# Performance work log

Hardware: AMD Instinct MI355X
Metric: run time of the kernel (lower is better)

Reference implementation:

```python
import jax, jax.numpy as jnp
import numpy as np

INPUT_SIZE = 608
STRIDE = 32
NUM_CLASSES = 20
NMS_THRESH = 0.5
NUM_ANCHOR = 5
ANCHORS = np.array([[1.19, 1.98], [2.79, 4.59], [4.53, 8.92], [8.06, 5.29], [10.32, 10.65]], dtype=np.float32)


def _conv(x, w, b, pad):
    # x: NCHW, w: OIHW
    y = jax.lax.conv_general_dilated(x, w, (1, 1), [(pad, pad), (pad, pad)],
                                     dimension_numbers=('NCHW', 'OIHW', 'NCHW'))
    return y + b[None, :, None, None]


def _leaky(x):
    return jnp.where(x > 0, x, 0.1 * x)


def _reorg(x, s=2):
    # space-to-depth, darknet reorg: [B,C,H,W] -> [B,C*s*s,H/s,W/s]
    B, C, H, W = x.shape
    x = x.reshape(B, C, H // s, s, W // s, s)
    x = x.transpose(0, 3, 5, 1, 2, 4)
    return x.reshape(B, C * s * s, H // s, W // s)


def _forward_boxes_scores(feat_layer2, feat_layer3, w1a, b1a, w1b, b1b, wr, br, w2, b2, wp, bp):
    p5 = _leaky(_conv(feat_layer3, w1a, b1a, 1))
    p5 = _leaky(_conv(p5, w1b, b1b, 1))
    p4 = _reorg(_leaky(_conv(feat_layer2, wr, br, 0)))         # [1,256,19,19]
    p5 = jnp.concatenate([p4, p5], axis=1)                      # [1,1280,19,19]
    p5 = _leaky(_conv(p5, w2, b2, 1))
    pred = _conv(p5, wp, bp, 0)                                 # [1,125,19,19]
    B, C, H, W = pred.shape
    pred = pred.transpose(0, 2, 3, 1).reshape(B, H * W, C)
    conf = pred[:, :, :NUM_ANCHOR].reshape(B, H * W * NUM_ANCHOR, 1)
    cls = pred[:, :, NUM_ANCHOR:(1 + NUM_CLASSES) * NUM_ANCHOR].reshape(B, H * W * NUM_ANCHOR, NUM_CLASSES)
    reg = pred[:, :, (1 + NUM_CLASSES) * NUM_ANCHOR:].reshape(B, H * W, NUM_ANCHOR, 4)
    # decode_xywh
    gy, gx = jnp.meshgrid(jnp.arange(H), jnp.arange(W), indexing='ij')
    grid = jnp.stack([gx, gy], axis=-1).astype(pred.dtype).reshape(1, H * W, 1, 2)
    anchor_wh = jnp.asarray(ANCHORS).reshape(1, 1, NUM_ANCHOR, 2)
    xy = jax.nn.sigmoid(reg[..., :2]) + grid
    wh = jnp.exp(reg[..., 2:]) * anchor_wh
    xywh = jnp.concatenate([xy, wh], axis=-1).reshape(B, -1, 4) * STRIDE
    boxes = jnp.concatenate([xywh[..., :2] - 0.5 * xywh[..., 2:],
                             xywh[..., :2] + 0.5 * xywh[..., 2:]], axis=-1)
    boxes = jnp.clip(boxes[0] / INPUT_SIZE, 0.0, 1.0)           # [N,4]
    scores = jax.nn.sigmoid(conf[0]) * jax.nn.softmax(cls[0], axis=-1)  # [N,20]
    return boxes, scores


def _per_class_nms(boxes, scores, class_mask):
    # greedy sequential NMS, faithful to the torch while-loop (suppress iff IoU > thresh)
    N = boxes.shape[0]
    s = jnp.where(class_mask, scores, -jnp.inf)
    order = jnp.argsort(-s)
    b = boxes[order]
    valid = class_mask[order]
    x1, y1, x2, y2 = b[:, 0], b[:, 1], b[:, 2], b[:, 3]
    areas = (x2 - x1) * (y2 - y1)
    iw = jnp.maximum(1e-10, jnp.minimum(x2[:, None], x2[None, :]) - jnp.maximum(x1[:, None], x1[None, :]))
    ih = jnp.maximum(1e-10, jnp.minimum(y2[:, None], y2[None, :]) - jnp.maximum(y1[:, None], y1[None, :]))
    inter = iw * ih
    iou = inter / (areas[:, None] + areas[None, :] - inter)
    upper = jnp.arange(N)[None, :] > jnp.arange(N)[:, None]
    sup_mat = (iou > NMS_THRESH) & upper

    def body(i, state):
        suppressed, keep = state
        cur = valid[i] & jnp.logical_not(suppressed[i])
        keep = keep.at[i].set(cur)
        suppressed = suppressed | (cur & sup_mat[i])
        return suppressed, keep

    _, keep_sorted = jax.lax.fori_loop(0, N, body, (jnp.zeros(N, bool), jnp.zeros(N, bool)))
    return jnp.zeros(N, bool).at[order].set(keep_sorted)


def setup_inputs() -> dict:
    key = jax.random.key(0)
    ks = jax.random.split(key, 8)
    w = lambda k, shape: jax.random.normal(k, shape, jnp.float32) * 0.01
    return {
        'feat_layer2': jax.random.normal(ks[0], (1, 512, 38, 38), jnp.float32),
        'feat_layer3': jax.random.normal(ks[1], (1, 1024, 19, 19), jnp.float32),
        'w1a': w(ks[2], (1024, 1024, 3, 3)), 'b1a': jnp.zeros((1024,), jnp.float32),
        'w1b': w(ks[3], (1024, 1024, 3, 3)), 'b1b': jnp.zeros((1024,), jnp.float32),
        'wr': w(ks[4], (64, 512, 1, 1)), 'br': jnp.zeros((64,), jnp.float32),
        'w2': w(ks[5], (1024, 1280, 3, 3)), 'b2': jnp.zeros((1024,), jnp.float32),
        'wp': w(ks[6], (125, 1024, 1, 1)), 'bp': jnp.zeros((125,), jnp.float32),
    }


def reference(feat_layer2, feat_layer3, w1a, b1a, w1b, b1b, wr, br, w2, b2, wp, bp):
    boxes, scores_full = _forward_boxes_scores(feat_layer2, feat_layer3,
                                               w1a, b1a, w1b, b1b, wr, br, w2, b2, wp, bp)
    cls_inds = jnp.argmax(scores_full, axis=1)                          # [N]
    scores = jnp.take_along_axis(scores_full, cls_inds[:, None], axis=1)[:, 0]
    masks = cls_inds[None, :] == jnp.arange(NUM_CLASSES)[:, None]       # [20,N]
    keeps = jax.vmap(lambda m: _per_class_nms(boxes, scores, m))(masks)
    keep = jnp.any(keeps, axis=0)                                       # [N] bool, fixed-shape mask
    return boxes, scores, cls_inds, keep
```

## Files before the change

kernel.cpp:

```cpp
#include <hip/hip_runtime.h>

typedef _Float16 f16;
typedef _Float16 f16x8 __attribute__((ext_vector_type(8)));
typedef float f32x4 __attribute__((ext_vector_type(4)));

#define N_BOX 1805
#define NPIX 361
#define NCLS 20
#define GNW 29
#define MB_ROWS 226

__device__ __forceinline__ float leakyf(float x){ return x > 0.f ? x : 0.1f*x; }
__device__ __forceinline__ float sigmoidf_(float x){ return 1.f/(1.f + expf(-x)); }

__global__ void transpose_k(const float* __restrict__ src, float* __restrict__ dst, int R, int C){
  int i = blockIdx.x*256 + threadIdx.x;
  if (i < R*C){ int r = i / C, c = i % C; dst[c*R + r] = src[i]; }
}

__global__ void wprep_k(const float* __restrict__ w, f16* __restrict__ whi, f16* __restrict__ wlo,
                        int Cin, int total){
  int i = blockIdx.x*256 + threadIdx.x;
  if (i >= total) return;
  int co = i / Cin, ci = i - co*Cin;
  const float* src = w + (size_t)i*9;
  int K9 = 9*Cin;
  size_t dbase = (size_t)co*K9 + ci;
  #pragma unroll
  for (int t = 0; t < 9; ++t){
    float v = src[t]*64.f;
    f16 hi = (f16)v;
    f16 lo = (f16)(v - (float)hi);
    whi[dbase + (size_t)t*Cin] = hi;
    wlo[dbase + (size_t)t*Cin] = lo;
  }
}

__global__ void act1prep_k(const float* __restrict__ feat3, f16* __restrict__ ah, f16* __restrict__ al){
  int i = blockIdx.x*256 + threadIdx.x;
  if (i >= NPIX*1024) return;
  int p = i >> 10, c = i & 1023;
  float v = feat3[c*NPIX + p];
  f16 hi = (f16)v; f16 lo = (f16)(v - (float)hi);
  ah[i] = hi; al[i] = lo;
}

__global__ __launch_bounds__(256) void reorg_conv_k(const float* __restrict__ feat2,
    const float* __restrict__ wrT, const float* __restrict__ br,
    f16* __restrict__ cath, f16* __restrict__ catl){
  int c  = threadIdx.x & 63;
  int pq = threadIdx.x >> 6;
  int pix = blockIdx.x*4 + pq;
  int y = pix / 38, x = pix % 38;
  __shared__ float s_in[64][4];
  float acc = br[c];
  for (int cb = 0; cb < 512; cb += 64){
    __syncthreads();
    { int k = threadIdx.x >> 2, pp = threadIdx.x & 3;
      s_in[k][pp] = feat2[(cb + k)*1444 + blockIdx.x*4 + pp]; }
    __syncthreads();
    #pragma unroll
    for (int k = 0; k < 64; ++k)
      acc = fmaf(wrT[(cb+k)*64 + c], s_in[k][pq], acc);
  }
  float v = leakyf(acc);
  int co = ((y & 1)*2 + (x & 1))*64 + c;
  int p = (y>>1)*19 + (x>>1);
  f16 hi = (f16)v; f16 lo = (f16)(v - (float)hi);
  size_t o = (size_t)p*1280 + co;
  cath[o] = hi; catl[o] = lo;
}

__global__ __launch_bounds__(256) void conv_mfma_k(
    const f16* __restrict__ whi, const f16* __restrict__ wlo,
    const f16* __restrict__ ahi, const f16* __restrict__ alo,
    float* __restrict__ part, int Cin, int chunks, int cpt)
{
  const int K9 = 9*Cin;
  int cob = blockIdx.x * 128;
  int px0 = blockIdx.y * 128;
  int ks  = blockIdx.z;
  int kc0 = ks * chunks;
  int tid = threadIdx.x;

  __shared__ f16 sAh[128*32], sAl[128*32], sBh[128*32], sBl[128*32];

  int r = tid >> 1, h = tid & 1;
  int wb0 = ((r*64 + h*32)      ) ^ ((r&7)<<4);
  int wb1 = ((r*64 + h*32 + 16) ) ^ ((r&7)<<4);
  const f16* wArowh = whi + (size_t)(cob + r)*K9 + h*16;
  const f16* wArowl = wlo + (size_t)(cob + r)*K9 + h*16;
  int p = px0 + r;
  int py = p / 19, px = p - py*19;

  int lane = tid & 63, wid = tid >> 6;
  int lrow = lane & 15, lgrp = lane >> 4;
  int wr = wid >> 1, wc = wid & 1;
  int swz = (lrow & 7) << 4;
  int aoff[4], boff[4];
  #pragma unroll
  for (int m = 0; m < 4; ++m){
    int rA = wr*64 + m*16 + lrow;
    aoff[m] = (rA*64 + lgrp*16) ^ swz;
    int rB = wc*64 + m*16 + lrow;
    boff[m] = (rB*64 + lgrp*16) ^ swz;
  }

  f32x4 acc[4][4] = {};

  for (int kc = kc0; kc < kc0 + chunks; ++kc){
    int t = kc / cpt;
    int ci0 = (kc - t*cpt) * 32;
    int dy = t / 3, dx = t - dy*3;
    int yy = py + dy - 1, xx = px + dx - 1;
    bool bvalid = (p < NPIX) && ((unsigned)yy < 19u) && ((unsigned)xx < 19u);

    f16x8 a0 = *(const f16x8*)(wArowh + (size_t)kc*32);
    f16x8 a1 = *(const f16x8*)(wArowh + (size_t)kc*32 + 8);
    f16x8 a2 = *(const f16x8*)(wArowl + (size_t)kc*32);
    f16x8 a3 = *(const f16x8*)(wArowl + (size_t)kc*32 + 8);
    f16x8 b0 = {}, b1 = {}, b2 = {}, b3 = {};
    if (bvalid){
      const f16* bh_src = ahi + (size_t)(yy*19+xx)*Cin + ci0 + h*16;
      const f16* bl_src = alo + (size_t)(yy*19+xx)*Cin + ci0 + h*16;
      b0 = *(const f16x8*)(bh_src);
      b1 = *(const f16x8*)(bh_src + 8);
      b2 = *(const f16x8*)(bl_src);
      b3 = *(const f16x8*)(bl_src + 8);
    }
    __syncthreads();
    *(f16x8*)((char*)sAh + wb0) = a0; *(f16x8*)((char*)sAh + wb1) = a1;
    *(f16x8*)((char*)sAl + wb0) = a2; *(f16x8*)((char*)sAl + wb1) = a3;
    *(f16x8*)((char*)sBh + wb0) = b0; *(f16x8*)((char*)sBh + wb1) = b1;
    *(f16x8*)((char*)sBl + wb0) = b2; *(f16x8*)((char*)sBl + wb1) = b3;
    __syncthreads();

    f16x8 bh[4], bl[4];
    #pragma unroll
    for (int n = 0; n < 4; ++n){
      bh[n] = *(const f16x8*)((char*)sBh + boff[n]);
      bl[n] = *(const f16x8*)((char*)sBl + boff[n]);
    }
    #pragma unroll
    for (int m = 0; m < 4; ++m){
      f16x8 ah = *(const f16x8*)((char*)sAh + aoff[m]);
      f16x8 al = *(const f16x8*)((char*)sAl + aoff[m]);
      #pragma unroll
      for (int n = 0; n < 4; ++n){
        acc[m][n] = __builtin_amdgcn_mfma_f32_16x16x32_f16(ah, bh[n], acc[m][n], 0,0,0);
        acc[m][n] = __builtin_amdgcn_mfma_f32_16x16x32_f16(ah, bl[n], acc[m][n], 0,0,0);
        acc[m][n] = __builtin_amdgcn_mfma_f32_16x16x32_f16(al, bh[n], acc[m][n], 0,0,0);
      }
    }
  }

  #pragma unroll
  for (int m = 0; m < 4; ++m){
    #pragma unroll
    for (int n = 0; n < 4; ++n){
      int pp = px0 + wc*64 + n*16 + lrow;
      if (pp < NPIX){
        int co = cob + wr*64 + m*16 + lgrp*4;
        size_t base = ((size_t)ks*1024 + co)*NPIX + pp;
        part[base          ] = acc[m][n][0];
        part[base +   NPIX ] = acc[m][n][1];
        part[base + 2*NPIX ] = acc[m][n][2];
        part[base + 3*NPIX ] = acc[m][n][3];
      }
    }
  }
}

__global__ void reduce16v_k(const float* __restrict__ part, const float* __restrict__ bias,
                            f16* __restrict__ dhi, f16* __restrict__ dlo,
                            int Cstride, int Coff, int splitk){
  int i = blockIdx.x*256 + threadIdx.x;
  if (i >= 1024*NPIX) return;
  int co = i / NPIX, p = i - co*NPIX;
  float s = 0.f;
  for (int k = 0; k < splitk; ++k) s += part[(size_t)k*1024*NPIX + i];
  float v = leakyf(s*0.015625f + bias[co]);
  f16 hi = (f16)v;
  f16 lo = (f16)(v - (float)hi);
  size_t o = (size_t)p*Cstride + Coff + co;
  dhi[o] = hi; dlo[o] = lo;
}

__global__ __launch_bounds__(256) void pred_conv_k(const f16* __restrict__ a3h, const f16* __restrict__ a3l,
    const float* __restrict__ wpT, const float* __restrict__ bp, float* __restrict__ pred){
  int c = threadIdx.x & 127, ph = threadIdx.x >> 7;
  int pix = blockIdx.x*2 + ph;
  __shared__ float s_in[64][2];
  float acc = 0.f;
  for (int cb = 0; cb < 1024; cb += 64){
    __syncthreads();
    if (threadIdx.x < 128){
      int k = threadIdx.x & 63, pp = threadIdx.x >> 6;
      int px2 = blockIdx.x*2 + pp;
      float v = 0.f;
      if (px2 < NPIX){
        size_t o = (size_t)px2*1024 + cb + k;
        v = (float)a3h[o] + (float)a3l[o];
      }
      s_in[k][pp] = v;
    }
    __syncthreads();
    if (c < 125){
      #pragma unroll
      for (int k = 0; k < 64; ++k)
        acc = fmaf(wpT[(cb+k)*125 + c], s_in[k][ph], acc);
    }
  }
  if (c < 125 && pix < NPIX) pred[c*NPIX + pix] = acc + bp[c];
}

__device__ const float ANCW[5] = {1.19f, 2.79f, 4.53f, 8.06f, 10.32f};
__device__ const float ANCH_[5] = {1.98f, 4.59f, 8.92f, 5.29f, 10.65f};

__global__ void decode_k(const float* __restrict__ pred, float* __restrict__ out,
                         int* __restrict__ cls_i, int* __restrict__ cnt){
  int n = blockIdx.x*256 + threadIdx.x;
  if (blockIdx.x == 0 && threadIdx.x < NCLS) cnt[threadIdx.x] = 0;
  if (n >= N_BOX) return;
  int p = n / 5, a = n % 5;
  float conf = pred[a*NPIX + p];
  float cl[20]; float m = -1e30f;
  #pragma unroll
  for (int k = 0; k < 20; ++k){ cl[k] = pred[(5 + a*20 + k)*NPIX + p]; m = fmaxf(m, cl[k]); }
  float s = 0.f;
  #pragma unroll
  for (int k = 0; k < 20; ++k){ cl[k] = expf(cl[k]-m); s += cl[k]; }
  int bi = 0; float bv = cl[0];
  #pragma unroll
  for (int k = 1; k < 20; ++k) if (cl[k] > bv){ bv = cl[k]; bi = k; }
  float score = sigmoidf_(conf) * (bv / s);
  float tx = pred[(105 + a*4 + 0)*NPIX + p];
  float ty = pred[(105 + a*4 + 1)*NPIX + p];
  float tw = pred[(105 + a*4 + 2)*NPIX + p];
  float th = pred[(105 + a*4 + 3)*NPIX + p];
  float gx = (float)(p % 19), gy = (float)(p / 19);
  float cx = (sigmoidf_(tx) + gx) * 32.f;
  float cy = (sigmoidf_(ty) + gy) * 32.f;
  float bw = expf(tw) * ANCW[a] * 32.f;
  float bh = expf(th) * ANCH_[a] * 32.f;
  float x1 = fminf(fmaxf((cx - 0.5f*bw) / 608.f, 0.f), 1.f);
  float y1 = fminf(fmaxf((cy - 0.5f*bh) / 608.f, 0.f), 1.f);
  float x2 = fminf(fmaxf((cx + 0.5f*bw) / 608.f, 0.f), 1.f);
  float y2 = fminf(fmaxf((cy + 0.5f*bh) / 608.f, 0.f), 1.f);
  out[n*4+0]=x1; out[n*4+1]=y1; out[n*4+2]=x2; out[n*4+3]=y2;
  out[7220 + n]  = score;
  out[9025 + n]  = (float)bi;
  out[10830 + n] = 0.f;
  cls_i[n] = bi;
}

__global__ __launch_bounds__(256) void rank_k(const float* __restrict__ scores,
    const int* __restrict__ cls_i, int* __restrict__ ord, int* __restrict__ cnt){
  __shared__ float s_sc[N_BOX];
  __shared__ short s_cl[N_BOX];
  int tid = threadIdx.x;
  for (int j = tid; j < N_BOX; j += 256){ s_sc[j] = scores[j]; s_cl[j] = (short)cls_i[j]; }
  __syncthreads();
  int wid = tid >> 6, lane = tid & 63;
  int i = blockIdx.x*4 + wid;
  if (i >= N_BOX) return;
  float si = s_sc[i]; short ci = s_cl[i];
  int r = 0;
  for (int j = lane; j < N_BOX; j += 64){
    float sj = s_sc[j];
    r += (int)((s_cl[j] == ci) & ((sj > si) | ((sj == si) & (j < i))));
  }
  #pragma unroll
  for (int o = 32; o; o >>= 1) r += __shfl_down(r, o);
  if (lane == 0){
    ord[ci*N_BOX + r] = i;
    atomicAdd(&cnt[ci], 1);
  }
}

__global__ __launch_bounds__(256) void maskbuild_k(const float* __restrict__ boxes,
    const int* __restrict__ ord, const int* __restrict__ cnt,
    unsigned long long* __restrict__ gmask){
  __shared__ float X1[N_BOX], Y1[N_BOX], X2[N_BOX], Y2[N_BOX], AR[N_BOX];
  int c = blockIdx.x, chunk = blockIdx.y, tid = threadIdx.x;
  int n = cnt[c];
  int r0 = chunk*MB_ROWS;
  if (n <= 0 || r0 >= n) return;
  int r1 = r0 + MB_ROWS; if (r1 > n) r1 = n;
  int rows_here = r1 - r0;
  for (int t = tid; t < n; t += 256){
    int bi = ord[c*N_BOX + t];
    float x1 = boxes[bi*4+0], y1 = boxes[bi*4+1], x2 = boxes[bi*4+2], y2 = boxes[bi*4+3];
    X1[t]=x1; Y1[t]=y1; X2[t]=x2; Y2[t]=y2; AR[t]=(x2-x1)*(y2-y1);
  }
  __syncthreads();
  int nw = (n + 63) >> 6;
  unsigned long long* rows = gmask + (size_t)c*N_BOX*GNW;
  for (int task = tid; task < rows_here*nw; task += 256){
    int w = task / rows_here, ri = task - w*rows_here;
    int i = r0 + ri;
    float ax1=X1[i], ay1=Y1[i], ax2=X2[i], ay2=Y2[i], areaA=AR[i];
    unsigned long long bits = 0;
    int j0 = w << 6;
    int jb = i+1 > j0 ? i+1 : j0;
    int je = j0+64 < n ? j0+64 : n;
    for (int j = jb; j < je; ++j){
      float iw = fmaxf(1e-10f, fminf(ax2,X2[j]) - fmaxf(ax1,X1[j]));
      float ih = fmaxf(1e-10f, fminf(ay2,Y2[j]) - fmaxf(ay1,Y1[j]));
      float inter = iw*ih;
      float iou = inter / (areaA + AR[j] - inter);
      bits |= (unsigned long long)(iou > 0.5f) << (j - j0);
    }
    rows[(size_t)i*GNW + w] = bits;
  }
}

__global__ __launch_bounds__(64) void nmsscan_k(const int* __restrict__ ord,
    const int* __restrict__ cnt, const unsigned long long* __restrict__ gmask,
    float* __restrict__ keep){
  __shared__ int sidx[N_BOX];
  int c = blockIdx.x, lane = threadIdx.x;
  int n = cnt[c];
  if (n <= 0) return;
  int nw = (n + 63) >> 6;
  for (int t = lane; t < n; t += 64) sidx[t] = ord[c*N_BOX + t];
  __syncthreads();
  const unsigned long long* rows = gmask + (size_t)c*N_BOX*GNW;
  bool act = lane < nw;
  unsigned long long S = 0;
  unsigned long long diag = (lane < n) ? rows[(size_t)lane*GNW + 0] : 0ull;
  for (int w = 0; w < nw; ++w){
    int base = w << 6;
    int nb = n - base; if (nb > 64) nb = 64;
    unsigned int slo = (unsigned)__builtin_amdgcn_readlane((int)(unsigned)S, w);
    unsigned int shi = (unsigned)__builtin_amdgcn_readlane((int)(unsigned)(S >> 32), w);
    unsigned long long sup = ((unsigned long long)shi << 32) | slo;
    unsigned long long validm = (nb >= 64) ? ~0ull : ((1ull << nb) - 1ull);
    unsigned long long avail = ~sup & validm;
    unsigned long long kmask = 0;
    unsigned long long diag_next = 0;
    if (w+1 < nw){
      int i2 = base + 64 + lane;
      if (i2 < n) diag_next = rows[(size_t)i2*GNW + (w+1)];
    }
    while (avail){
      int b = __builtin_ctzll(avail);
      kmask |= 1ull << b;
      unsigned int dlo = (unsigned)__builtin_amdgcn_readlane((int)(unsigned)diag, b);
      unsigned int dhi = (unsigned)__builtin_amdgcn_readlane((int)(unsigned)(diag >> 32), b);
      unsigned long long drow = ((unsigned long long)dhi << 32) | dlo;
      sup |= drow;
      avail &= ~(1ull << b);
      avail &= ~sup;
      if (act && lane > w)
        S |= rows[(size_t)(base + b)*GNW + lane];
    }
    if ((kmask >> lane) & 1ull) keep[sidx[base + lane]] = 1.f;
    diag = diag_next;
  }
}

static inline size_t align256(size_t x){ return (x + 255) & ~(size_t)255; }

extern "C" void kernel_launch(void* const* d_in, const int* in_sizes, int n_in,
                              void* d_out, int out_size, void* d_ws, size_t ws_size,
                              hipStream_t stream){
  const float* feat2 = (const float*)d_in[0];
  const float* feat3 = (const float*)d_in[1];
  const float* w1a = (const float*)d_in[2];
  const float* b1a = (const float*)d_in[3];
  const float* w1b = (const float*)d_in[4];
  const float* b1b = (const float*)d_in[5];
  const float* wr  = (const float*)d_in[6];
  const float* br  = (const float*)d_in[7];
  const float* w2  = (const float*)d_in[8];
  const float* b2  = (const float*)d_in[9];
  const float* wp  = (const float*)d_in[10];
  const float* bp  = (const float*)d_in[11];
  float* out = (float*)d_out;
  char* ws = (char*)d_ws;

  size_t off = 0;
  float* part = (float*)(ws + off); off = align256(off + (size_t)16*1024*NPIX*4);
  f16* wh   = (f16*)(ws + off); off = align256(off + (size_t)1024*1280*9*2);
  f16* wl   = (f16*)(ws + off); off = align256(off + (size_t)1024*1280*9*2);
  f16* a1h  = (f16*)(ws + off); off = align256(off + (size_t)NPIX*1024*2);
  f16* a1l  = (f16*)(ws + off); off = align256(off + (size_t)NPIX*1024*2);
  f16* a2h  = (f16*)(ws + off); off = align256(off + (size_t)NPIX*1024*2);
  f16* a2l  = (f16*)(ws + off); off = align256(off + (size_t)NPIX*1024*2);
  f16* a3h  = (f16*)(ws + off); off = align256(off + (size_t)NPIX*1024*2);
  f16* a3l  = (f16*)(ws + off); off = align256(off + (size_t)NPIX*1024*2);
  f16* cath = (f16*)(ws + off); off = align256(off + (size_t)NPIX*1280*2);
  f16* catl = (f16*)(ws + off); off = align256(off + (size_t)NPIX*1280*2);
  float* pred = (float*)(ws + off); off = align256(off + (size_t)125*NPIX*4);
  float* wrT  = (float*)(ws + off); off = align256(off + (size_t)512*64*4);
  float* wpT  = (float*)(ws + off); off = align256(off + (size_t)1024*125*4);
  int* cls_i  = (int*)(ws + off); off = align256(off + (size_t)N_BOX*4);
  int* ord    = (int*)(ws + off); off = align256(off + (size_t)NCLS*N_BOX*4);
  int* cnt    = (int*)(ws + off); off = align256(off + (size_t)NCLS*4);
  unsigned long long* gmask = (unsigned long long*)part;

  transpose_k<<<(64*512 + 255)/256, 256, 0, stream>>>(wr, wrT, 64, 512);
  transpose_k<<<(125*1024 + 255)/256, 256, 0, stream>>>(wp, wpT, 125, 1024);
  act1prep_k<<<(NPIX*1024 + 255)/256, 256, 0, stream>>>(feat3, a1h, a1l);
  reorg_conv_k<<<361, 256, 0, stream>>>(feat2, wrT, br, cath, catl);

  wprep_k<<<(1024*1024 + 255)/256, 256, 0, stream>>>(w1a, wh, wl, 1024, 1024*1024);
  { dim3 g(8, 3, 16);
    conv_mfma_k<<<g, 256, 0, stream>>>(wh, wl, a1h, a1l, part, 1024, 18, 32); }
  reduce16v_k<<<(1024*NPIX + 255)/256, 256, 0, stream>>>(part, b1a, a2h, a2l, 1024, 0, 16);

  wprep_k<<<(1024*1024 + 255)/256, 256, 0, stream>>>(w1b, wh, wl, 1024, 1024*1024);
  { dim3 g(8, 3, 16);
    conv_mfma_k<<<g, 256, 0, stream>>>(wh, wl, a2h, a2l, part, 1024, 18, 32); }
  reduce16v_k<<<(1024*NPIX + 255)/256, 256, 0, stream>>>(part, b1b, cath, catl, 1280, 256, 16);

  wprep_k<<<(1024*1280 + 255)/256, 256, 0, stream>>>(w2, wh, wl, 1280, 1024*1280);
  { dim3 g(8, 3, 15);
    conv_mfma_k<<<g, 256, 0, stream>>>(wh, wl, cath, catl, part, 1280, 24, 40); }
  reduce16v_k<<<(1024*NPIX + 255)/256, 256, 0, stream>>>(part, b2, a3h, a3l, 1024, 0, 15);

  pred_conv_k<<<181, 256, 0, stream>>>(a3h, a3l, wpT, bp, pred);
  decode_k<<<8, 256, 0, stream>>>(pred, out, cls_i, cnt);
  rank_k<<<(N_BOX + 3)/4, 256, 0, stream>>>(out + 7220, cls_i, ord, cnt);
  { dim3 mg(NCLS, 8);
    maskbuild_k<<<mg, 256, 0, stream>>>(out, ord, cnt, gmask); }
  nmsscan_k<<<NCLS, 64, 0, stream>>>(ord, cnt, gmask, out + 10830);
}
```

Baseline: 318.2 us.

## Double-buffer conv MFMA shared tiles and raise split-K to 24

The conv MFMA kernel now keeps two shared-memory buffers and prefetches the next K-chunk's global loads into registers while the current chunk's MFMAs run, so each iteration needs one barrier instead of two. Hi/lo halves are merged into one 128-wide row per tile, and each thread now loads a full 32-element hi or lo row. Split-K goes from 16/15 to 24 slices, giving 576 blocks per conv, with a larger partial buffer and a longer reduction in exchange. The doubled LDS footprint (64 KB) may reduce occupancy.

```diff
diff --git a/kernel.cpp b/kernel.cpp
--- a/kernel.cpp
+++ b/kernel.cpp
@@ -83,68 +83,88 @@
   int kc0 = ks * chunks;
   int tid = threadIdx.x;
 
-  __shared__ f16 sAh[128*32], sAl[128*32], sBh[128*32], sBl[128*32];
+  __shared__ f16 sA[2][128*64];
+  __shared__ f16 sB[2][128*64];
 
   int r = tid >> 1, h = tid & 1;
-  int wb0 = ((r*64 + h*32)      ) ^ ((r&7)<<4);
-  int wb1 = ((r*64 + h*32 + 16) ) ^ ((r&7)<<4);
-  const f16* wArowh = whi + (size_t)(cob + r)*K9 + h*16;
-  const f16* wArowl = wlo + (size_t)(cob + r)*K9 + h*16;
+  int wboff[4];
+  #pragma unroll
+  for (int j = 0; j < 4; ++j)
+    wboff[j] = (r*128 + (h*4 + j)*16) ^ ((r & 7) << 4);
+
+  const f16* wArow = (h ? wlo : whi) + (size_t)(cob + r)*K9;
   int p = px0 + r;
   int py = p / 19, px = p - py*19;
+  const f16* bbase = (h ? alo : ahi);
 
   int lane = tid & 63, wid = tid >> 6;
   int lrow = lane & 15, lgrp = lane >> 4;
   int wr = wid >> 1, wc = wid & 1;
-  int swz = (lrow & 7) << 4;
-  int aoff[4], boff[4];
+  int aoffH[4], aoffL[4], boffH[4], boffL[4];
   #pragma unroll
   for (int m = 0; m < 4; ++m){
     int rA = wr*64 + m*16 + lrow;
-    aoff[m] = (rA*64 + lgrp*16) ^ swz;
+    aoffH[m] = (rA*128 + lgrp*16)     ^ ((rA & 7) << 4);
+    aoffL[m] = (rA*128 + (4+lgrp)*16) ^ ((rA & 7) << 4);
     int rB = wc*64 + m*16 + lrow;
-    boff[m] = (rB*64 + lgrp*16) ^ swz;
+    boffH[m] = (rB*128 + lgrp*16)     ^ ((rB & 7) << 4);
+    boffL[m] = (rB*128 + (4+lgrp)*16) ^ ((rB & 7) << 4);
   }
 
   f32x4 acc[4][4] = {};
-
-  for (int kc = kc0; kc < kc0 + chunks; ++kc){
+  f16x8 sa0, sa1, sa2, sa3, sb0, sb1, sb2, sb3;
+
+  auto LOADK = [&](int kc){
+    const f16* as = wArow + (size_t)kc*32;
+    sa0 = *(const f16x8*)(as);
+    sa1 = *(const f16x8*)(as + 8);
+    sa2 = *(const f16x8*)(as + 16);
+    sa3 = *(const f16x8*)(as + 24);
     int t = kc / cpt;
     int ci0 = (kc - t*cpt) * 32;
-    int dy = t / 3, dx = t - dy*3;
+    int dy = t/3, dx = t - dy*3;
     int yy = py + dy - 1, xx = px + dx - 1;
     bool bvalid = (p < NPIX) && ((unsigned)yy < 19u) && ((unsigned)xx < 19u);
-
-    f16x8 a0 = *(const f16x8*)(wArowh + (size_t)kc*32);
-    f16x8 a1 = *(const f16x8*)(wArowh + (size_t)kc*32 + 8);
-    f16x8 a2 = *(const f16x8*)(wArowl + (size_t)kc*32);
-    f16x8 a3 = *(const f16x8*)(wArowl + (size_t)kc*32 + 8);
-    f16x8 b0 = {}, b1 = {}, b2 = {}, b3 = {};
+    f16x8 z = {};
+    sb0 = z; sb1 = z; sb2 = z; sb3 = z;
     if (bvalid){
-      const f16* bh_src = ahi + (size_t)(yy*19+xx)*Cin + ci0 + h*16;
-      const f16* bl_src = alo + (size_t)(yy*19+xx)*Cin + ci0 + h*16;
-      b0 = *(const f16x8*)(bh_src);
-      b1 = *(const f16x8*)(bh_src + 8);
-      b2 = *(const f16x8*)(bl_src);
-      b3 = *(const f16x8*)(bl_src + 8);
-    }
-    __syncthreads();
-    *(f16x8*)((char*)sAh + wb0) = a0; *(f16x8*)((char*)sAh + wb1) = a1;
-    *(f16x8*)((char*)sAl + wb0) = a2; *(f16x8*)((char*)sAl + wb1) = a3;
-    *(f16x8*)((char*)sBh + wb0) = b0; *(f16x8*)((char*)sBh + wb1) = b1;
-    *(f16x8*)((char*)sBl + wb0) = b2; *(f16x8*)((char*)sBl + wb1) = b3;
-    __syncthreads();
+      const f16* bs = bbase + (size_t)(yy*19+xx)*Cin + ci0;
+      sb0 = *(const f16x8*)(bs);
+      sb1 = *(const f16x8*)(bs + 8);
+      sb2 = *(const f16x8*)(bs + 16);
+      sb3 = *(const f16x8*)(bs + 24);
+    }
+  };
+  auto WRITEK = [&](int buf){
+    *(f16x8*)((char*)sA[buf] + wboff[0]) = sa0;
+    *(f16x8*)((char*)sA[buf] + wboff[1]) = sa1;
+    *(f16x8*)((char*)sA[buf] + wboff[2]) = sa2;
+    *(f16x8*)((char*)sA[buf] + wboff[3]) = sa3;
+    *(f16x8*)((char*)sB[buf] + wboff[0]) = sb0;
+    *(f16x8*)((char*)sB[buf] + wboff[1]) = sb1;
+    *(f16x8*)((char*)sB[buf] + wboff[2]) = sb2;
+    *(f16x8*)((char*)sB[buf] + wboff[3]) = sb3;
+  };
+
+  LOADK(kc0);
+  WRITEK(0);
+  __syncthreads();
+
+  for (int i = 0; i < chunks; ++i){
+    int cur = i & 1;
+    bool more = (i + 1 < chunks);
+    if (more) LOADK(kc0 + i + 1);
 
     f16x8 bh[4], bl[4];
     #pragma unroll
     for (int n = 0; n < 4; ++n){
-      bh[n] = *(const f16x8*)((char*)sBh + boff[n]);
-      bl[n] = *(const f16x8*)((char*)sBl + boff[n]);
+      bh[n] = *(const f16x8*)((char*)sB[cur] + boffH[n]);
+      bl[n] = *(const f16x8*)((char*)sB[cur] + boffL[n]);
     }
     #pragma unroll
     for (int m = 0; m < 4; ++m){
-      f16x8 ah = *(const f16x8*)((char*)sAh + aoff[m]);
-      f16x8 al = *(const f16x8*)((char*)sAl + aoff[m]);
+      f16x8 ah = *(const f16x8*)((char*)sA[cur] + aoffH[m]);
+      f16x8 al = *(const f16x8*)((char*)sA[cur] + aoffL[m]);
       #pragma unroll
       for (int n = 0; n < 4; ++n){
         acc[m][n] = __builtin_amdgcn_mfma_f32_16x16x32_f16(ah, bh[n], acc[m][n], 0,0,0);
@@ -152,6 +172,8 @@
         acc[m][n] = __builtin_amdgcn_mfma_f32_16x16x32_f16(al, bh[n], acc[m][n], 0,0,0);
       }
     }
+    if (more) WRITEK(cur ^ 1);
+    __syncthreads();
   }
 
   #pragma unroll
@@ -381,7 +403,7 @@
   char* ws = (char*)d_ws;
 
   size_t off = 0;
-  float* part = (float*)(ws + off); off = align256(off + (size_t)16*1024*NPIX*4);
+  float* part = (float*)(ws + off); off = align256(off + (size_t)24*1024*NPIX*4);
   f16* wh   = (f16*)(ws + off); off = align256(off + (size_t)1024*1280*9*2);
   f16* wl   = (f16*)(ws + off); off = align256(off + (size_t)1024*1280*9*2);
   f16* a1h  = (f16*)(ws + off); off = align256(off + (size_t)NPIX*1024*2);
@@ -406,19 +428,19 @@
   reorg_conv_k<<<361, 256, 0, stream>>>(feat2, wrT, br, cath, catl);
 
   wprep_k<<<(1024*1024 + 255)/256, 256, 0, stream>>>(w1a, wh, wl, 1024, 1024*1024);
-  { dim3 g(8, 3, 16);
-    conv_mfma_k<<<g, 256, 0, stream>>>(wh, wl, a1h, a1l, part, 1024, 18, 32); }
-  reduce16v_k<<<(1024*NPIX + 255)/256, 256, 0, stream>>>(part, b1a, a2h, a2l, 1024, 0, 16);
+  { dim3 g(8, 3, 24);
+    conv_mfma_k<<<g, 256, 0, stream>>>(wh, wl, a1h, a1l, part, 1024, 12, 32); }
+  reduce16v_k<<<(1024*NPIX + 255)/256, 256, 0, stream>>>(part, b1a, a2h, a2l, 1024, 0, 24);
 
   wprep_k<<<(1024*1024 + 255)/256, 256, 0, stream>>>(w1b, wh, wl, 1024, 1024*1024);
-  { dim3 g(8, 3, 16);
-    conv_mfma_k<<<g, 256, 0, stream>>>(wh, wl, a2h, a2l, part, 1024, 18, 32); }
-  reduce16v_k<<<(1024*NPIX + 255)/256, 256, 0, stream>>>(part, b1b, cath, catl, 1280, 256, 16);
+  { dim3 g(8, 3, 24);
+    conv_mfma_k<<<g, 256, 0, stream>>>(wh, wl, a2h, a2l, part, 1024, 12, 32); }
+  reduce16v_k<<<(1024*NPIX + 255)/256, 256, 0, stream>>>(part, b1b, cath, catl, 1280, 256, 24);
 
   wprep_k<<<(1024*1280 + 255)/256, 256, 0, stream>>>(w2, wh, wl, 1280, 1024*1280);
-  { dim3 g(8, 3, 15);
-    conv_mfma_k<<<g, 256, 0, stream>>>(wh, wl, cath, catl, part, 1280, 24, 40); }
-  reduce16v_k<<<(1024*NPIX + 255)/256, 256, 0, stream>>>(part, b2, a3h, a3l, 1024, 0, 15);
+  { dim3 g(8, 3, 24);
+    conv_mfma_k<<<g, 256, 0, stream>>>(wh, wl, cath, catl, part, 1280, 15, 40); }
+  reduce16v_k<<<(1024*NPIX + 255)/256, 256, 0, stream>>>(part, b2, a3h, a3l, 1024, 0, 24);
 
   pred_conv_k<<<181, 256, 0, stream>>>(a3h, a3l, wpT, bp, pred);
   decode_k<<<8, 256, 0, stream>>>(pred, out, cls_i, cnt);
```

Result: slower. 350.2 us (+10.0%).
